# Performance work log

Measured on AMD Instinct MI355X. Metric: run time of the kernel, lower is better.

Reference implementation:

```python
import jax, jax.numpy as jnp
import numpy as np

N_NODES = 100000
N_EDGES = 1600000
IN_CH = 256
OUT_CH = 32
HEADS = 4
NEG_SLOPE = 0.2


def setup_inputs() -> dict:
    key = jax.random.key(0)
    k1, k2, k3, k4, k5 = jax.random.split(key, 5)
    x = jax.random.normal(k1, (N_NODES, IN_CH), dtype=jnp.float32)
    edge_index = jax.random.randint(k2, (2, N_EDGES), 0, N_NODES, dtype=jnp.int64)
    hc = HEADS * OUT_CH
    # glorot init like the torch module
    std_w = np.sqrt(6.0 / (hc + IN_CH))
    W = jax.random.uniform(k3, (hc, IN_CH), dtype=jnp.float32, minval=-std_w, maxval=std_w)
    b = jnp.zeros((hc,), dtype=jnp.float32)
    std_a = np.sqrt(6.0 / (hc + 2))
    att = jax.random.uniform(k4, (hc, 2), dtype=jnp.float32, minval=-std_a, maxval=std_a)
    return {"x": x, "edge_index": edge_index, "W": W, "b": b, "att": att}


def reference(x, edge_index, W, b, att):
    # flow = 'target_to_source': tid=0, sid=1
    tar = edge_index[0]
    src = edge_index[1]
    feat = x @ W.T + b                      # [N, H*C]
    e_pre = feat @ att                      # [N, 2]
    e_src = e_pre[:, 0:1]                   # [N, 1]
    e_tar = e_pre[:, 1:2]                   # [N, 1]
    # edge scores
    e = jnp.exp(jax.nn.leaky_relu(e_src[src] + e_tar[tar], negative_slope=NEG_SLOPE))   # [E, 1]
    e_self = jnp.exp(jax.nn.leaky_relu(e_src + e_tar, negative_slope=NEG_SLOPE))        # [N, 1]
    # softmax denominator over incoming edges + self loop
    e_sum = jax.ops.segment_sum(e, tar, num_segments=N_NODES) + e_self                  # [N, 1]
    alpha_self = e_self / e_sum             # [N, 1]
    alpha = e / e_sum[tar]                  # [E, 1]
    # weighted aggregation (dropout=0 / eval -> identity)
    out = jax.ops.segment_sum(feat[src] * alpha, tar, num_segments=N_NODES)
    out = out + feat * alpha_self           # [N, H*C], concat=True
    return out
```

## Files before the change

kernel.cpp:

```cpp
#include <hip/hip_runtime.h>
#include <hip/hip_bf16.h>
#include <math.h>

#define N_NODES 100000
#define N_EDGES 1600000
#define IN_CH 256
#define HC 128
#define NEG_SLOPE 0.2f

#define NB_C 196
#define CCAP 8704
#define CHUNK 3200

#define GBM 128
#define GEMM_BLOCKS 782
#define BIN_BLOCKS 500

typedef __attribute__((ext_vector_type(8))) short short8;
typedef __attribute__((ext_vector_type(4))) float floatx4;

__device__ inline ushort f2b(float f) {
    __hip_bfloat16 h = __float2bfloat16(f);
    return *(ushort*)&h;
}

__device__ inline float edge_e(float z) {
    float lr = z > 0.f ? z : NEG_SLOPE * z;
    return __expf(lr);
}

__device__ inline float bflo(unsigned u) { return __uint_as_float(u << 16); }
__device__ inline float bfhi(unsigned u) { return __uint_as_float(u & 0xffff0000u); }

__global__ __launch_bounds__(256)
void wconv_k(const float* __restrict__ W, ushort* __restrict__ wb) {
    int i = blockIdx.x * 256 + threadIdx.x;
    float4 v = *(const float4*)&W[(size_t)i * 4];
    ushort4 u;
    u.x = f2b(v.x); u.y = f2b(v.y); u.z = f2b(v.z); u.w = f2b(v.w);
    *(ushort4*)&wb[(size_t)i * 4] = u;
}

__global__ __launch_bounds__(256, 2)
void fused_gemm_bin_k(const float* __restrict__ x, const ushort* __restrict__ wb,
                      const float* __restrict__ b, const float* __restrict__ att,
                      __hip_bfloat16* __restrict__ featb,
                      float* __restrict__ e_src, float* __restrict__ e_tar,
                      float* __restrict__ e_self,
                      const int* __restrict__ ei, int* __restrict__ gcur,
                      int* __restrict__ ebuf) {
    __shared__ ushort xs[128][72];
    __shared__ ushort wsh[128][72];
    __shared__ int lcnt[NB_C];
    __shared__ int lcur[NB_C];

    const int tid = threadIdx.x;

    if (blockIdx.x >= GEMM_BLOCKS) {
        const int base = (blockIdx.x - GEMM_BLOCKS) * CHUNK;

        for (int i = tid; i < NB_C; i += 256) lcnt[i] = 0;
        __syncthreads();

        for (int i = tid; i < CHUNK; i += 256)
            atomicAdd(&lcnt[ei[base + i] >> 9], 1);
        __syncthreads();

        for (int bkt = tid; bkt < NB_C; bkt += 256) {
            int c = lcnt[bkt];
            lcur[bkt] = c ? atomicAdd(&gcur[bkt], c) : 0;
        }
        __syncthreads();

        for (int i = tid; i < CHUNK; i += 256) {
            int t = ei[base + i];
            int s = ei[N_EDGES + base + i];
            int bkt = t >> 9;
            int pos = atomicAdd(&lcur[bkt], 1);
            if (pos < CCAP)
                ebuf[bkt * CCAP + pos] = s | ((t & 511) << 17);
        }
        return;
    }

    const int wave = tid >> 6;
    const int lane = tid & 63;
    const int l16  = lane >> 4;
    const int lc   = lane & 15;
    const int row0 = blockIdx.x * GBM;

    floatx4 acc[2][8];
    #pragma unroll
    for (int mt = 0; mt < 2; ++mt)
        #pragma unroll
        for (int nt = 0; nt < 8; ++nt)
            acc[mt][nt] = (floatx4){0.f, 0.f, 0.f, 0.f};

    const int r  = tid >> 4;
    const int kq = tid & 15;

    for (int kb = 0; kb < 4; ++kb) {
        float4 xv[8];
        #pragma unroll
        for (int i = 0; i < 8; ++i) {
            int gr = row0 + r + i * 16;
            int grc = gr < N_NODES ? gr : N_NODES - 1;
            xv[i] = *(const float4*)&x[(size_t)grc * IN_CH + kb * 64 + kq * 4];
        }
        ushort4 wv[8];
        #pragma unroll
        for (int i = 0; i < 8; ++i)
            wv[i] = *(const ushort4*)&wb[(size_t)(r + i * 16) * IN_CH + kb * 64 + kq * 4];

        #pragma unroll
        for (int i = 0; i < 8; ++i) {
            ushort4 u;
            u.x = f2b(xv[i].x); u.y = f2b(xv[i].y);
            u.z = f2b(xv[i].z); u.w = f2b(xv[i].w);
            *(ushort4*)&xs[r + i * 16][kq * 4] = u;
        }
        #pragma unroll
        for (int i = 0; i < 8; ++i)
            *(ushort4*)&wsh[r + i * 16][kq * 4] = wv[i];

        __syncthreads();
        #pragma unroll
        for (int ks = 0; ks < 2; ++ks) {
            short8 a0 = *(short8*)&xs[wave * 32 + lc][ks * 32 + l16 * 8];
            short8 a1 = *(short8*)&xs[wave * 32 + 16 + lc][ks * 32 + l16 * 8];
            short8 bf[8];
            #pragma unroll
            for (int nt = 0; nt < 8; ++nt)
                bf[nt] = *(short8*)&wsh[nt * 16 + lc][ks * 32 + l16 * 8];
            #pragma unroll
            for (int nt = 0; nt < 8; ++nt) {
                acc[0][nt] = __builtin_amdgcn_mfma_f32_16x16x32_bf16(a0, bf[nt], acc[0][nt], 0, 0, 0);
                acc[1][nt] = __builtin_amdgcn_mfma_f32_16x16x32_bf16(a1, bf[nt], acc[1][nt], 0, 0, 0);
            }
        }
        __syncthreads();
    }

    float av0[8], av1[8], bc[8];
    #pragma unroll
    for (int nt = 0; nt < 8; ++nt) {
        float2 av = *(const float2*)&att[(nt * 16 + lc) * 2];
        av0[nt] = av.x; av1[nt] = av.y;
        bc[nt] = b[nt * 16 + lc];
    }

    #pragma unroll
    for (int mt = 0; mt < 2; ++mt) {
        #pragma unroll
        for (int rg = 0; rg < 4; ++rg) {
            int row = row0 + wave * 32 + mt * 16 + l16 * 4 + rg;
            float s = 0.f, t = 0.f;
            float vals[8];
            #pragma unroll
            for (int nt = 0; nt < 8; ++nt) {
                float v = acc[mt][nt][rg] + bc[nt];
                vals[nt] = v;
                s += v * av0[nt];
                t += v * av1[nt];
            }
            #pragma unroll
            for (int off = 8; off; off >>= 1) {
                s += __shfl_xor(s, off);
                t += __shfl_xor(t, off);
            }
            if (row < N_NODES) {
                if (lc == 0) {
                    e_src[row] = s;
                    e_tar[row] = t;
                    float z = s + t;
                    float lr = z > 0.f ? z : NEG_SLOPE * z;
                    e_self[row] = __expf(lr);
                }
                #pragma unroll
                for (int nt = 0; nt < 8; ++nt)
                    featb[(size_t)row * HC + nt * 16 + lc] = __float2bfloat16(vals[nt]);
            }
        }
    }
}

__global__ __launch_bounds__(512)
void bucket_csr2_k(const int* __restrict__ gcur, const int* __restrict__ ebuf,
                   const float* __restrict__ e_src, const float* __restrict__ e_tar,
                   int* __restrict__ offsets, int* __restrict__ csr_src,
                   float* __restrict__ ewb) {
    const int b = blockIdx.x;
    const int tid = threadIdx.x;

    __shared__ int sc[256];
    __shared__ int lcnt[512];
    __shared__ int lofs[512];
    __shared__ int lout[CCAP];
    __shared__ float ltar[512];

    {
        int n = b * 512 + tid;
        ltar[tid] = (n < N_NODES) ? e_tar[n] : 0.f;
    }

    if (tid < 256) {
        int c = 0;
        if (tid < NB_C) { c = gcur[tid]; if (c > CCAP) c = CCAP; }
        sc[tid] = c;
    }
    lcnt[tid] = 0;
    __syncthreads();
    #pragma unroll
    for (int off = 1; off < 256; off <<= 1) {
        int v = 0;
        if (tid < 256) v = sc[tid] + ((tid >= off) ? sc[tid - off] : 0);
        __syncthreads();
        if (tid < 256) sc[tid] = v;
        __syncthreads();
    }
    int count = gcur[b]; if (count > CCAP) count = CCAP;
    const int base = (b == 0) ? 0 : sc[b - 1];

    const int* st = &ebuf[b * CCAP];
    for (int i = tid; i < count; i += 512)
        atomicAdd(&lcnt[st[i] >> 17], 1);
    __syncthreads();

    lofs[tid] = lcnt[tid];
    __syncthreads();
    for (int off = 1; off < 512; off <<= 1) {
        int v = lofs[tid] + ((tid >= off) ? lofs[tid - off] : 0);
        __syncthreads();
        lofs[tid] = v;
        __syncthreads();
    }
    int excl = lofs[tid] - lcnt[tid];
    lcnt[tid] = excl;

    {
        int n0 = b * 512 + tid;
        if (n0 < N_NODES) offsets[n0] = base + excl;
    }
    if (b == NB_C - 1 && tid == 0) offsets[N_NODES] = base + count;
    __syncthreads();

    for (int i = tid; i < count; i += 512) {
        int v = st[i];
        int pos = atomicAdd(&lcnt[v >> 17], 1);
        lout[pos] = v;
    }
    __syncthreads();

    for (int i = tid; i < count; i += 512) {
        int v = lout[i];
        int src = v & 0x1FFFF;
        csr_src[base + i] = src;
        ewb[base + i] = edge_e(e_src[src] + ltar[v >> 17]);
    }
}

__global__ __launch_bounds__(256)
void aggregate_k(const int* __restrict__ offsets, const int* __restrict__ csr_src,
                 const float* __restrict__ ewb,
                 const __hip_bfloat16* __restrict__ featb,
                 const float* __restrict__ e_self, float* __restrict__ out) {
    int node = blockIdx.x * 4 + (threadIdx.x >> 6);
    if (node >= N_NODES) return;
    int lane = threadIdx.x & 63;
    int g = lane >> 4;
    int q = lane & 15;
    int beg = offsets[node];
    int end = offsets[node + 1];
    float eself = e_self[node];

    const char* fb = (const char*)featb;
    const size_t qofs = (size_t)(q * 16);

    uint4 su = *(const uint4*)(fb + (size_t)node * 256 + qofs);
    float m0 = (g == 0) ? eself : 0.f;
    float esum = m0;
    float acc[8];
    acc[0] = m0 * bflo(su.x); acc[1] = m0 * bfhi(su.x);
    acc[2] = m0 * bflo(su.y); acc[3] = m0 * bfhi(su.y);
    acc[4] = m0 * bflo(su.z); acc[5] = m0 * bfhi(su.z);
    acc[6] = m0 * bflo(su.w); acc[7] = m0 * bfhi(su.w);

    int j = beg;
    for (; j + 7 < end; j += 8) {
        int s0 = csr_src[j + g];
        int s1 = csr_src[j + 4 + g];
        float e0 = ewb[j + g];
        float e1 = ewb[j + 4 + g];
        uint4 u0 = *(const uint4*)(fb + (size_t)s0 * 256 + qofs);
        uint4 u1 = *(const uint4*)(fb + (size_t)s1 * 256 + qofs);
        esum += e0 + e1;
        acc[0] += e0 * bflo(u0.x) + e1 * bflo(u1.x);
        acc[1] += e0 * bfhi(u0.x) + e1 * bfhi(u1.x);
        acc[2] += e0 * bflo(u0.y) + e1 * bflo(u1.y);
        acc[3] += e0 * bfhi(u0.y) + e1 * bfhi(u1.y);
        acc[4] += e0 * bflo(u0.z) + e1 * bflo(u1.z);
        acc[5] += e0 * bfhi(u0.z) + e1 * bfhi(u1.z);
        acc[6] += e0 * bflo(u0.w) + e1 * bflo(u1.w);
        acc[7] += e0 * bfhi(u0.w) + e1 * bfhi(u1.w);
    }
    for (; j + 3 < end; j += 4) {
        int s0 = csr_src[j + g];
        float e0 = ewb[j + g];
        uint4 u0 = *(const uint4*)(fb + (size_t)s0 * 256 + qofs);
        esum += e0;
        acc[0] += e0 * bflo(u0.x);
        acc[1] += e0 * bfhi(u0.x);
        acc[2] += e0 * bflo(u0.y);
        acc[3] += e0 * bfhi(u0.y);
        acc[4] += e0 * bflo(u0.z);
        acc[5] += e0 * bfhi(u0.z);
        acc[6] += e0 * bflo(u0.w);
        acc[7] += e0 * bfhi(u0.w);
    }
    for (; j < end; ++j) {
        int s0 = csr_src[j];
        float ew = ewb[j];
        uint4 u0 = *(const uint4*)(fb + (size_t)s0 * 256 + qofs);
        float em = (g == 0) ? ew : 0.f;
        esum += em;
        acc[0] += em * bflo(u0.x);
        acc[1] += em * bfhi(u0.x);
        acc[2] += em * bflo(u0.y);
        acc[3] += em * bfhi(u0.y);
        acc[4] += em * bflo(u0.z);
        acc[5] += em * bfhi(u0.z);
        acc[6] += em * bflo(u0.w);
        acc[7] += em * bfhi(u0.w);
    }

    #pragma unroll
    for (int k = 0; k < 8; ++k) {
        acc[k] += __shfl_xor(acc[k], 16);
        acc[k] += __shfl_xor(acc[k], 32);
    }
    esum += __shfl_xor(esum, 16);
    esum += __shfl_xor(esum, 32);

    if (g == 0) {
        float inv = 1.f / esum;
        float* op = &out[(size_t)node * HC + q * 8];
        *(float4*)op = make_float4(acc[0] * inv, acc[1] * inv, acc[2] * inv, acc[3] * inv);
        *(float4*)(op + 4) = make_float4(acc[4] * inv, acc[5] * inv, acc[6] * inv, acc[7] * inv);
    }
}

extern "C" void kernel_launch(void* const* d_in, const int* in_sizes, int n_in,
                              void* d_out, int out_size, void* d_ws, size_t ws_size,
                              hipStream_t stream) {
    const float* x   = (const float*)d_in[0];
    const int*   ei  = (const int*)d_in[1];
    const float* W   = (const float*)d_in[2];
    const float* b   = (const float*)d_in[3];
    const float* att = (const float*)d_in[4];
    float* out = (float*)d_out;

    unsigned char* p = (unsigned char*)d_ws;
    auto take = [&](size_t bytes) {
        unsigned char* r = p;
        p += (bytes + 255) & ~(size_t)255;
        return (void*)r;
    };
    __hip_bfloat16* featb = (__hip_bfloat16*)take((size_t)N_NODES * HC * sizeof(__hip_bfloat16));
    float* e_src   = (float*)take((size_t)N_NODES * sizeof(float));
    float* e_tar   = (float*)take((size_t)N_NODES * sizeof(float));
    float* e_self  = (float*)take((size_t)N_NODES * sizeof(float));
    int*   offsets = (int*)take((size_t)(N_NODES + 1) * sizeof(int));
    int*   gcur    = (int*)take((size_t)NB_C * sizeof(int));
    int*   csr_src = (int*)take((size_t)N_EDGES * sizeof(int));
    float* ewb     = (float*)take((size_t)N_EDGES * sizeof(float));
    int*   ebuf    = (int*)take((size_t)NB_C * CCAP * sizeof(int));
    ushort* wb     = (ushort*)take((size_t)HC * IN_CH * sizeof(ushort));

    (void)hipMemsetAsync(gcur, 0, NB_C * sizeof(int), stream);

    wconv_k<<<(HC * IN_CH) / (256 * 4), 256, 0, stream>>>(W, wb);

    fused_gemm_bin_k<<<GEMM_BLOCKS + BIN_BLOCKS, 256, 0, stream>>>(
        x, wb, b, att, featb, e_src, e_tar, e_self, ei, gcur, ebuf);

    bucket_csr2_k<<<NB_C, 512, 0, stream>>>(gcur, ebuf, e_src, e_tar,
                                            offsets, csr_src, ewb);

    aggregate_k<<<(N_NODES + 3) / 4, 256, 0, stream>>>(offsets, csr_src, ewb,
                                                       featb, e_self, out);
}
```

Measured before the change: 294.7 us.

## Replace bucketed two-level CSR build with degree histogram, single-block scan, atomic scatter

```diff
diff --git a/kernel.cpp b/kernel.cpp
--- a/kernel.cpp
+++ b/kernel.cpp
@@ -8,13 +8,11 @@
 #define HC 128
 #define NEG_SLOPE 0.2f
 
-#define NB_C 196
-#define CCAP 8704
 #define CHUNK 3200
 
 #define GBM 128
 #define GEMM_BLOCKS 782
-#define BIN_BLOCKS 500
+#define HIST_BLOCKS 500
 
 typedef __attribute__((ext_vector_type(8))) short short8;
 typedef __attribute__((ext_vector_type(4))) float floatx4;
@@ -42,44 +40,21 @@
 }
 
 __global__ __launch_bounds__(256, 2)
-void fused_gemm_bin_k(const float* __restrict__ x, const ushort* __restrict__ wb,
-                      const float* __restrict__ b, const float* __restrict__ att,
-                      __hip_bfloat16* __restrict__ featb,
-                      float* __restrict__ e_src, float* __restrict__ e_tar,
-                      float* __restrict__ e_self,
-                      const int* __restrict__ ei, int* __restrict__ gcur,
-                      int* __restrict__ ebuf) {
+void fused_gemm_hist_k(const float* __restrict__ x, const ushort* __restrict__ wb,
+                       const float* __restrict__ b, const float* __restrict__ att,
+                       __hip_bfloat16* __restrict__ featb,
+                       float* __restrict__ e_src, float* __restrict__ e_tar,
+                       float* __restrict__ e_self,
+                       const int* __restrict__ ei, int* __restrict__ deg) {
     __shared__ ushort xs[128][72];
     __shared__ ushort wsh[128][72];
-    __shared__ int lcnt[NB_C];
-    __shared__ int lcur[NB_C];
 
     const int tid = threadIdx.x;
 
     if (blockIdx.x >= GEMM_BLOCKS) {
         const int base = (blockIdx.x - GEMM_BLOCKS) * CHUNK;
-
-        for (int i = tid; i < NB_C; i += 256) lcnt[i] = 0;
-        __syncthreads();
-
         for (int i = tid; i < CHUNK; i += 256)
-            atomicAdd(&lcnt[ei[base + i] >> 9], 1);
-        __syncthreads();
-
-        for (int bkt = tid; bkt < NB_C; bkt += 256) {
-            int c = lcnt[bkt];
-            lcur[bkt] = c ? atomicAdd(&gcur[bkt], c) : 0;
-        }
-        __syncthreads();
-
-        for (int i = tid; i < CHUNK; i += 256) {
-            int t = ei[base + i];
-            int s = ei[N_EDGES + base + i];
-            int bkt = t >> 9;
-            int pos = atomicAdd(&lcur[bkt], 1);
-            if (pos < CCAP)
-                ebuf[bkt * CCAP + pos] = s | ((t & 511) << 17);
-        }
+            atomicAdd(&deg[ei[base + i]], 1);
         return;
     }
 
@@ -184,78 +159,72 @@
     }
 }
 
-__global__ __launch_bounds__(512)
-void bucket_csr2_k(const int* __restrict__ gcur, const int* __restrict__ ebuf,
-                   const float* __restrict__ e_src, const float* __restrict__ e_tar,
-                   int* __restrict__ offsets, int* __restrict__ csr_src,
-                   float* __restrict__ ewb) {
-    const int b = blockIdx.x;
-    const int tid = threadIdx.x;
-
-    __shared__ int sc[256];
-    __shared__ int lcnt[512];
-    __shared__ int lofs[512];
-    __shared__ int lout[CCAP];
-    __shared__ float ltar[512];
-
-    {
-        int n = b * 512 + tid;
-        ltar[tid] = (n < N_NODES) ? e_tar[n] : 0.f;
-    }
-
-    if (tid < 256) {
-        int c = 0;
-        if (tid < NB_C) { c = gcur[tid]; if (c > CCAP) c = CCAP; }
-        sc[tid] = c;
-    }
-    lcnt[tid] = 0;
+#define SCAN_TILE 8192
+
+__global__ __launch_bounds__(1024)
+void scan_k(const int* __restrict__ deg, int* __restrict__ offsets,
+            int* __restrict__ cur) {
+    __shared__ int tile[SCAN_TILE];
+    __shared__ int part[1024];
+    __shared__ int carry;
+    const int t = threadIdx.x;
+    if (t == 0) carry = 0;
     __syncthreads();
-    #pragma unroll
-    for (int off = 1; off < 256; off <<= 1) {
-        int v = 0;
-        if (tid < 256) v = sc[tid] + ((tid >= off) ? sc[tid - off] : 0);
-        __syncthreads();
-        if (tid < 256) sc[tid] = v;
-        __syncthreads();
-    }
-    int count = gcur[b]; if (count > CCAP) count = CCAP;
-    const int base = (b == 0) ? 0 : sc[b - 1];
-
-    const int* st = &ebuf[b * CCAP];
-    for (int i = tid; i < count; i += 512)
-        atomicAdd(&lcnt[st[i] >> 17], 1);
-    __syncthreads();
-
-    lofs[tid] = lcnt[tid];
-    __syncthreads();
-    for (int off = 1; off < 512; off <<= 1) {
-        int v = lofs[tid] + ((tid >= off) ? lofs[tid - off] : 0);
-        __syncthreads();
-        lofs[tid] = v;
-        __syncthreads();
-    }
-    int excl = lofs[tid] - lcnt[tid];
-    lcnt[tid] = excl;
-
-    {
-        int n0 = b * 512 + tid;
-        if (n0 < N_NODES) offsets[n0] = base + excl;
-    }
-    if (b == NB_C - 1 && tid == 0) offsets[N_NODES] = base + count;
-    __syncthreads();
-
-    for (int i = tid; i < count; i += 512) {
-        int v = st[i];
-        int pos = atomicAdd(&lcnt[v >> 17], 1);
-        lout[pos] = v;
-    }
-    __syncthreads();
-
-    for (int i = tid; i < count; i += 512) {
-        int v = lout[i];
-        int src = v & 0x1FFFF;
-        csr_src[base + i] = src;
-        ewb[base + i] = edge_e(e_src[src] + ltar[v >> 17]);
+
+    for (int t0 = 0; t0 < N_NODES; t0 += SCAN_TILE) {
+        int n = N_NODES - t0; if (n > SCAN_TILE) n = SCAN_TILE;
+
+        for (int i = t; i < SCAN_TILE; i += 1024)
+            tile[i] = (i < n) ? deg[t0 + i] : 0;
+        __syncthreads();
+
+        const int e0 = t * 8;
+        int loc[8];
+        int s = 0;
+        #pragma unroll
+        for (int k = 0; k < 8; ++k) {
+            loc[k] = s;
+            s += tile[e0 + k];
+        }
+        part[t] = s;
+        __syncthreads();
+
+        for (int off = 1; off < 1024; off <<= 1) {
+            int v = part[t] + ((t >= off) ? part[t - off] : 0);
+            __syncthreads();
+            part[t] = v;
+            __syncthreads();
+        }
+        const int cbase = carry + part[t] - s;
+
+        #pragma unroll
+        for (int k = 0; k < 8; ++k) {
+            int idx = e0 + k;
+            if (idx < n) {
+                int o = cbase + loc[k];
+                offsets[t0 + idx] = o;
+                cur[t0 + idx] = o;
+            }
+        }
+        __syncthreads();
+        if (t == 0) carry += part[1023];
+        __syncthreads();
+    }
+    if (t == 0) offsets[N_NODES] = carry;
+}
+
+__global__ __launch_bounds__(256)
+void scatter_k(const int* __restrict__ ei, int* __restrict__ cur,
+               const float* __restrict__ e_src, const float* __restrict__ e_tar,
+               int* __restrict__ csr_src, float* __restrict__ ewb) {
+    int i0 = blockIdx.x * 256 + threadIdx.x;
+    int stride = gridDim.x * 256;
+    for (int i = i0; i < N_EDGES; i += stride) {
+        int t = ei[i];
+        int s = ei[N_EDGES + i];
+        int pos = atomicAdd(&cur[t], 1);
+        csr_src[pos] = s;
+        ewb[pos] = edge_e(e_src[s] + e_tar[t]);
     }
 }
 
@@ -370,21 +339,22 @@
     float* e_tar   = (float*)take((size_t)N_NODES * sizeof(float));
     float* e_self  = (float*)take((size_t)N_NODES * sizeof(float));
     int*   offsets = (int*)take((size_t)(N_NODES + 1) * sizeof(int));
-    int*   gcur    = (int*)take((size_t)NB_C * sizeof(int));
+    int*   deg     = (int*)take((size_t)N_NODES * sizeof(int));
+    int*   cur     = (int*)take((size_t)N_NODES * sizeof(int));
     int*   csr_src = (int*)take((size_t)N_EDGES * sizeof(int));
     float* ewb     = (float*)take((size_t)N_EDGES * sizeof(float));
-    int*   ebuf    = (int*)take((size_t)NB_C * CCAP * sizeof(int));
     ushort* wb     = (ushort*)take((size_t)HC * IN_CH * sizeof(ushort));
 
-    (void)hipMemsetAsync(gcur, 0, NB_C * sizeof(int), stream);
+    (void)hipMemsetAsync(deg, 0, N_NODES * sizeof(int), stream);
 
     wconv_k<<<(HC * IN_CH) / (256 * 4), 256, 0, stream>>>(W, wb);
 
-    fused_gemm_bin_k<<<GEMM_BLOCKS + BIN_BLOCKS, 256, 0, stream>>>(
-        x, wb, b, att, featb, e_src, e_tar, e_self, ei, gcur, ebuf);
-
-    bucket_csr2_k<<<NB_C, 512, 0, stream>>>(gcur, ebuf, e_src, e_tar,
-                                            offsets, csr_src, ewb);
+    fused_gemm_hist_k<<<GEMM_BLOCKS + HIST_BLOCKS, 256, 0, stream>>>(
+        x, wb, b, att, featb, e_src, e_tar, e_self, ei, deg);
+
+    scan_k<<<1, 1024, 0, stream>>>(deg, offsets, cur);
+
+    scatter_k<<<2048, 256, 0, stream>>>(ei, cur, e_src, e_tar, csr_src, ewb);
 
     aggregate_k<<<(N_NODES + 3) / 4, 256, 0, stream>>>(offsets, csr_src, ewb,
                                                        featb, e_self, out);
```

Result: slower. 534.4 us (+81.4%).
